# Kernel tuning notes

Measured on AMD Instinct MI355X. Metric: run time of the kernel, lower is better.

The kernel has to match this reference:

```python
import jax, jax.numpy as jnp
import numpy as np
from jax import lax


def setup_inputs() -> dict:
    key = jax.random.key(0)
    I = jax.random.uniform(key, (32, 3, 512, 512), dtype=jnp.float32)
    return {"I": I, "k": 15}


def reference(I, k):
    # Channel-wise min -> dark channel (torch does this via -max_pool over transposed channel dim)
    dark = jnp.min(I, axis=1, keepdims=True)  # [B,1,H,W]
    p = k // 2
    # Spatial min-pool kxk, stride 1, pad k//2. torch max_pool2d pads with -inf,
    # so the min-pool equivalent pads with +inf: reduce_window with min and +inf init.
    eroded = lax.reduce_window(
        dark,
        jnp.inf,
        lax.min,
        window_dimensions=(1, 1, k, k),
        window_strides=(1, 1, 1, 1),
        padding=[(0, 0), (0, 0), (p, p), (p, p)],
    )
    return eroded
```

## Files before the change

### kernel.cpp

```cpp
#include <hip/hip_runtime.h>
#include <math.h>

#define BATCH  32
#define CH     3
#define H      512
#define W      512
#define KWIN   15
#define PAD    7
#define TH     16
#define NRR    (TH + KWIN - 1)
#define STRIP  112
#define NSTRIP 5
#define NWAVES (BATCH * (H / TH) * NSTRIP)
#define DEPTH  5

static __device__ __forceinline__ float2 min2(float2 a, float2 b) {
    float2 r;
    r.x = fminf(a.x, b.x);
    r.y = fminf(a.y, b.y);
    return r;
}

__global__ void dcp_fused8(const float* __restrict__ I, float* __restrict__ out) {
    const int wid = blockIdx.x * 4 + (threadIdx.x >> 6);
    const int L   = threadIdx.x & 63;
    const int s   = wid % NSTRIP;
    const int rb  = (wid / NSTRIP) % (H / TH);
    const int b   = wid / (NSTRIP * (H / TH));
    const int y0  = rb * TH;
    const int f   = s * STRIP - 8 + 2 * L;
    const int cl  = min(max(f, 0), W - 2);
    const bool cv = (f >= 0) && (f < W);
    const bool st = (L >= 4) && (L <= 59) && (f < W);

    const float* base = I + (size_t)b * CH * H * W + cl;
    float* outb = out + (size_t)b * H * W;

    auto seqrow = [](int q) { return q < KWIN ? KWIN + q : 29 - q; };

    auto loadrow = [&](int i, float2& A, float2& B, float2& C) {
        const int yc = min(max(y0 - PAD + i, 0), H - 1);
        const float* p = base + (size_t)yc * W;
        A = *(const float2*)(p);
        B = *(const float2*)(p + (size_t)H * W);
        C = *(const float2*)(p + (size_t)2 * H * W);
    };

    auto hcompute = [&](int i, float2 A, float2 B, float2 C) -> float2 {
        const int y = y0 - PAD + i;
        float2 d = min2(min2(A, B), C);
        const bool pad = (y < 0) || (y >= H) || !cv;
        d.x = pad ? INFINITY : d.x;
        d.y = pad ? INFINITY : d.y;
        const float pm = fminf(d.x, d.y);
        const float t2 = fminf(pm, __shfl_down(pm, 1));
        const float t4 = fminf(t2, __shfl_down(t2, 2));
        const float q7 = fminf(t4, __shfl_up(t4, 3));
        float2 wv;
        wv.x = fminf(q7, __shfl_up(d.y, 4));
        wv.y = fminf(q7, __shfl_down(d.x, 4));
        return wv;
    };

    float2 Ab[DEPTH], Bb[DEPTH], Cb[DEPTH];
    #pragma unroll
    for (int j = 0; j < DEPTH; ++j)
        loadrow(seqrow(j), Ab[j], Bb[j], Cb[j]);

    float2 P[KWIN];
    float2 U;
    #pragma unroll
    for (int q = 0; q < NRR; ++q) {
        const int sl = q % DEPTH;
        const float2 h = hcompute(seqrow(q), Ab[sl], Bb[sl], Cb[sl]);
        if (q + DEPTH < NRR)
            loadrow(seqrow(q + DEPTH), Ab[sl], Bb[sl], Cb[sl]);

        if (q == 0) {
            P[0] = h;
        } else if (q < KWIN) {
            P[q] = min2(P[q - 1], h);
            if (q == KWIN - 1 && st)
                *(float2*)(outb + (size_t)(y0 + 15) * W + f) = P[KWIN - 1];
        } else if (q == KWIN) {
            U = h;
            if (st) *(float2*)(outb + (size_t)(y0 + 14) * W + f) = min2(U, P[13]);
        } else if (q < NRR - 1) {
            const int r = 29 - q;
            U = min2(U, h);
            if (st) *(float2*)(outb + (size_t)(y0 + r) * W + f) = min2(U, P[r - 1]);
        } else {
            U = min2(U, h);
            if (st) *(float2*)(outb + (size_t)y0 * W + f) = U;
        }
    }
}

extern "C" void kernel_launch(void* const* d_in, const int* in_sizes, int n_in,
                              void* d_out, int out_size, void* d_ws, size_t ws_size,
                              hipStream_t stream) {
    const float* I = (const float*)d_in[0];
    float* out = (float*)d_out;
    dcp_fused8<<<dim3(NWAVES / 4), dim3(256), 0, stream>>>(I, out);
}
```

Baseline: 159.9 us.

## Double row tile height and extend van Herk vertical min to cover 32 rows

Raises the number of output rows per wave from 16 to 32 and extends the vertical van Herk/Gil-Werman scheme: a suffix-min buffer over the first 15 rows serves the lower half of the tile, and a running prefix over the extra rows produces rows 16-31. The halo of 14 input rows is now shared over twice as many outputs, which cuts redundant global loads and horizontal-min work per output row. In exchange register pressure rises from the extra buffers, and the grid has half as many waves, which lowers parallelism.

```diff
diff --git a/kernel.cpp b/kernel.cpp
--- a/kernel.cpp
+++ b/kernel.cpp
@@ -7,8 +7,8 @@
 #define W      512
 #define KWIN   15
 #define PAD    7
-#define TH     16
-#define NRR    (TH + KWIN - 1)
+#define TH     32
+#define NRT    (TH + KWIN - 1)
 #define STRIP  112
 #define NSTRIP 5
 #define NWAVES (BATCH * (H / TH) * NSTRIP)
@@ -21,7 +21,7 @@
     return r;
 }
 
-__global__ void dcp_fused8(const float* __restrict__ I, float* __restrict__ out) {
+__global__ void dcp_fused9(const float* __restrict__ I, float* __restrict__ out) {
     const int wid = blockIdx.x * 4 + (threadIdx.x >> 6);
     const int L   = threadIdx.x & 63;
     const int s   = wid % NSTRIP;
@@ -36,7 +36,7 @@
     const float* base = I + (size_t)b * CH * H * W + cl;
     float* outb = out + (size_t)b * H * W;
 
-    auto seqrow = [](int q) { return q < KWIN ? KWIN + q : 29 - q; };
+    auto seqrow = [](int q) { return q < KWIN ? KWIN + q : (q < 2 * KWIN ? 29 - q : q); };
 
     auto loadrow = [&](int i, float2& A, float2& B, float2& C) {
         const int yc = min(max(y0 - PAD + i, 0), H - 1);
@@ -67,31 +67,48 @@
     for (int j = 0; j < DEPTH; ++j)
         loadrow(seqrow(j), Ab[j], Bb[j], Cb[j]);
 
-    float2 P[KWIN];
-    float2 U;
+    float2 hbuf[KWIN];
+    float2 P1[KWIN - 1];
+    float2 U, pp, pp31;
+
     #pragma unroll
-    for (int q = 0; q < NRR; ++q) {
+    for (int q = 0; q < NRT; ++q) {
         const int sl = q % DEPTH;
         const float2 h = hcompute(seqrow(q), Ab[sl], Bb[sl], Cb[sl]);
-        if (q + DEPTH < NRR)
+        if (q + DEPTH < NRT)
             loadrow(seqrow(q + DEPTH), Ab[sl], Bb[sl], Cb[sl]);
 
-        if (q == 0) {
-            P[0] = h;
-        } else if (q < KWIN) {
-            P[q] = min2(P[q - 1], h);
-            if (q == KWIN - 1 && st)
-                *(float2*)(outb + (size_t)(y0 + 15) * W + f) = P[KWIN - 1];
-        } else if (q == KWIN) {
-            U = h;
-            if (st) *(float2*)(outb + (size_t)(y0 + 14) * W + f) = min2(U, P[13]);
-        } else if (q < NRR - 1) {
+        if (q < KWIN) {
+            hbuf[q] = h;
+            if (q == 0)            P1[0] = h;
+            else if (q < KWIN - 1) P1[q] = min2(P1[q - 1], h);
+            if (q == KWIN - 1) {
+                #pragma unroll
+                for (int i = KWIN - 2; i >= 0; --i)
+                    hbuf[i] = min2(hbuf[i], hbuf[i + 1]);
+                if (st) *(float2*)(outb + (size_t)(y0 + 15) * W + f) = hbuf[0];
+            }
+        } else if (q < 2 * KWIN) {
             const int r = 29 - q;
-            U = min2(U, h);
-            if (st) *(float2*)(outb + (size_t)(y0 + r) * W + f) = min2(U, P[r - 1]);
+            U = (q == KWIN) ? h : min2(U, h);
+            if (st) {
+                if (r > 0)
+                    *(float2*)(outb + (size_t)(y0 + r) * W + f) = min2(U, P1[r - 1]);
+                else
+                    *(float2*)(outb + (size_t)y0 * W + f) = U;
+            }
         } else {
-            U = min2(U, h);
-            if (st) *(float2*)(outb + (size_t)y0 * W + f) = U;
+            const int j = q - 2 * KWIN;
+            pp = (j == 0) ? h : min2(pp, h);
+            if (j == 1)      pp31 = h;
+            else if (j > 1)  pp31 = min2(pp31, h);
+            if (j <= 13) {
+                if (st) *(float2*)(outb + (size_t)(y0 + 16 + j) * W + f) = min2(hbuf[j + 1], pp);
+            } else if (j == 14) {
+                if (st) *(float2*)(outb + (size_t)(y0 + 30) * W + f) = pp;
+            } else {
+                if (st) *(float2*)(outb + (size_t)(y0 + 31) * W + f) = pp31;
+            }
         }
     }
 }
@@ -101,5 +118,5 @@
                               hipStream_t stream) {
     const float* I = (const float*)d_in[0];
     float* out = (float*)d_out;
-    dcp_fused8<<<dim3(NWAVES / 4), dim3(256), 0, stream>>>(I, out);
+    dcp_fused9<<<dim3(NWAVES / 4), dim3(256), 0, stream>>>(I, out);
 }
```

New measurement: 264.8 us. +65.6%, slower.
